# Performance work log

Measured on AMD Instinct MI355X. Metric: run time of the kernel, lower is better.

## Reference

```python
import jax, jax.numpy as jnp
from jax import lax
import numpy as np

B, S, H, DIN, BIN, NH, NL = 32, 256, 256, 16, 2, 8, 3
DH = H // NH


def setup_inputs() -> dict:
    key = jax.random.key(0)
    it = iter(jax.random.split(key, 40))
    def nrm(shape, s=0.05):
        return jax.random.normal(next(it), shape, jnp.float32) * s
    return {
        "parts": jax.random.normal(next(it), (B, S, DIN), jnp.float32),
        "bin_info": jax.random.normal(next(it), (B, BIN), jnp.float32),
        "target": jax.random.randint(next(it), (B, S), 0, S, dtype=jnp.int32),
        "pe_W1": nrm((H // 2, DIN)), "pe_b1": jnp.zeros((H // 2,), jnp.float32),
        "pe_W2": nrm((H // 2, H // 2)), "pe_b2": jnp.zeros((H // 2,), jnp.float32),
        "be_W1": nrm((H // 4, BIN)), "be_b1": jnp.zeros((H // 4,), jnp.float32),
        "be_W2": nrm((H // 4, H // 4)), "be_b2": jnp.zeros((H // 4,), jnp.float32),
        "pos_emb": nrm((S, H // 4)),
        "tr_Wqkv": nrm((NL, 3 * H, H)), "tr_bqkv": jnp.zeros((NL, 3 * H), jnp.float32),
        "tr_Wo": nrm((NL, H, H)), "tr_bo": jnp.zeros((NL, H), jnp.float32),
        "tr_ln1_g": jnp.ones((NL, H), jnp.float32), "tr_ln1_b": jnp.zeros((NL, H), jnp.float32),
        "tr_ff_W1": nrm((NL, 2 * H, H)), "tr_ff_b1": jnp.zeros((NL, 2 * H), jnp.float32),
        "tr_ff_W2": nrm((NL, H, 2 * H)), "tr_ff_b2": jnp.zeros((NL, H), jnp.float32),
        "tr_ln2_g": jnp.ones((NL, H), jnp.float32), "tr_ln2_b": jnp.zeros((NL, H), jnp.float32),
        "lstm_Wih": nrm((4 * H, H)), "lstm_Whh": nrm((4 * H, H)),
        "lstm_bih": jnp.zeros((4 * H,), jnp.float32), "lstm_bhh": jnp.zeros((4 * H,), jnp.float32),
        "ptr_W": nrm((H, H)), "ptr_b": jnp.zeros((H,), jnp.float32),
        "ptr_v": nrm((H,)),
    }


def _ln(x, g, b):
    m = x.mean(-1, keepdims=True)
    v = ((x - m) ** 2).mean(-1, keepdims=True)
    return (x - m) / jnp.sqrt(v + 1e-5) * g + b


def _forward(parts, bin_info, target, pe_W1, pe_b1, pe_W2, pe_b2,
             be_W1, be_b1, be_W2, be_b2, pos_emb,
             tr_Wqkv, tr_bqkv, tr_Wo, tr_bo, tr_ln1_g, tr_ln1_b,
             tr_ff_W1, tr_ff_b1, tr_ff_W2, tr_ff_b2, tr_ln2_g, tr_ln2_b,
             lstm_Wih, lstm_Whh, lstm_bih, lstm_bhh, ptr_W, ptr_b, ptr_v):
    # --- encode_inputs (dropout inactive in eval) ---
    p = jax.nn.relu(parts @ pe_W1.T + pe_b1) @ pe_W2.T + pe_b2            # [B,S,H/2]
    bb = jax.nn.relu(bin_info @ be_W1.T + be_b1) @ be_W2.T + be_b2        # [B,H/4]
    bb = jnp.broadcast_to(bb[:, None, :], (B, S, H // 4))
    pe = jnp.broadcast_to(pos_emb[None], (B, S, H // 4))
    x = jnp.concatenate([p, bb, pe], axis=-1)                             # [B,S,H]
    scale = 1.0 / np.sqrt(DH)
    for l in range(NL):  # post-norm TransformerEncoderLayer, relu FFN
        qkv = x @ tr_Wqkv[l].T + tr_bqkv[l]
        q, k, v = jnp.split(qkv, 3, axis=-1)
        q = q.reshape(B, S, NH, DH).transpose(0, 2, 1, 3)
        k = k.reshape(B, S, NH, DH).transpose(0, 2, 1, 3)
        v = v.reshape(B, S, NH, DH).transpose(0, 2, 1, 3)
        a = jax.nn.softmax(jnp.einsum('bhqd,bhkd->bhqk', q, k) * scale, axis=-1)
        o = jnp.einsum('bhqk,bhkd->bhqd', a, v).transpose(0, 2, 1, 3).reshape(B, S, H)
        x = _ln(x + o @ tr_Wo[l].T + tr_bo[l], tr_ln1_g[l], tr_ln1_b[l])
        ff = jax.nn.relu(x @ tr_ff_W1[l].T + tr_ff_b1[l]) @ tr_ff_W2[l].T + tr_ff_b2[l]
        x = _ln(x + ff, tr_ln2_g[l], tr_ln2_b[l])
    enc = x
    # Note: the original's inner MultiheadAttention calls never feed the
    # returned step_logits (part_logit is overwritten), so the faithful output is
    # logits[b,t,i] = v . tanh(ptr(h_t) + ptr(enc_i)), vectorized over i here.
    e_proj = enc @ ptr_W.T + ptr_b                                        # [B,S,H]
    bidx = jnp.arange(B)

    def step(carry, tgt_t):
        h, c, xin = carry
        g = xin @ lstm_Wih.T + lstm_bih + h @ lstm_Whh.T + lstm_bhh
        i, f, gg, o = jnp.split(g, 4, axis=-1)
        c = jax.nn.sigmoid(f) * c + jax.nn.sigmoid(i) * jnp.tanh(gg)
        h = jax.nn.sigmoid(o) * jnp.tanh(c)
        hp = h @ ptr_W.T + ptr_b                                          # [B,H]
        logits = jnp.tanh(hp[:, None, :] + e_proj) @ ptr_v                # [B,S]
        nxt = enc[bidx, tgt_t]                                            # teacher forcing
        return (h, c, nxt), logits

    z = jnp.zeros((B, H), jnp.float32)
    _, logits = lax.scan(step, (z, z, z), target.T)                       # [S,B,S]
    return logits.transpose(1, 0, 2)                                      # [B,S,S]


def reference(parts, bin_info, target, pe_W1, pe_b1, pe_W2, pe_b2,
              be_W1, be_b1, be_W2, be_b2, pos_emb,
              tr_Wqkv, tr_bqkv, tr_Wo, tr_bo, tr_ln1_g, tr_ln1_b,
              tr_ff_W1, tr_ff_b1, tr_ff_W2, tr_ff_b2, tr_ln2_g, tr_ln2_b,
              lstm_Wih, lstm_Whh, lstm_bih, lstm_bhh, ptr_W, ptr_b, ptr_v):
    return _forward(parts, bin_info, target, pe_W1, pe_b1, pe_W2, pe_b2,
                    be_W1, be_b1, be_W2, be_b2, pos_emb,
                    tr_Wqkv, tr_bqkv, tr_Wo, tr_bo, tr_ln1_g, tr_ln1_b,
                    tr_ff_W1, tr_ff_b1, tr_ff_W2, tr_ff_b2, tr_ln2_g, tr_ln2_b,
                    lstm_Wih, lstm_Whh, lstm_bih, lstm_bhh, ptr_W, ptr_b, ptr_v)
```

## Files before the change

### kernel.cpp

```cpp
#include <hip/hip_runtime.h>
#include <cstddef>

#define DEV __device__ __forceinline__

DEV float fexp2(float x) { return __builtin_amdgcn_exp2f(x); }
DEV float frcp(float x)  { return __builtin_amdgcn_rcpf(x); }
DEV float fsigm(float x) { return frcp(1.0f + fexp2(-1.44269504f * x)); }
DEV float ftanh_(float x){ return 1.0f - 2.0f * frcp(1.0f + fexp2(2.88539008f * x)); }

typedef _Float16 h2t __attribute__((ext_vector_type(2)));
typedef _Float16 v8h __attribute__((ext_vector_type(8)));
typedef float v4f __attribute__((ext_vector_type(4)));
union U32H2 { unsigned int u; h2t h; };
DEV h2t u2h(unsigned int u) { U32H2 x; x.u = u; return x.h; }

template <int BM, int BN, bool RELU, bool OUTF16>
__global__ __launch_bounds__(256) void hgemm_kernel(
    const _Float16* __restrict__ A, const _Float16* __restrict__ W,
    const float* __restrict__ bias1, const float* __restrict__ bias2,
    void* __restrict__ Cout, int M, int N, int K)
{
    constexpr int MT = BM / 32;
    constexpr int NT = BN / 32;
    constexpr int RA = BM / 64;
    constexpr int RB = BN / 64;
    __shared__ _Float16 As[BM * 32];
    __shared__ _Float16 Bs[BN * 32];

    const int tid = threadIdx.x;
    const int lane = tid & 63;
    const int lm = lane & 15, lq = lane >> 4;
    const int wrow = ((tid >> 6) & 1) * (BM / 2);
    const int wcol = (tid >> 7) * (BN / 2);
    const int m0 = blockIdx.x * BM, n0 = blockIdx.y * BN;
    const _Float16* Ab = A + (size_t)m0 * K;
    const _Float16* Wb = W + (size_t)n0 * K;

    v4f acc[MT][NT];
#pragma unroll
    for (int i = 0; i < MT; ++i)
#pragma unroll
        for (int j = 0; j < NT; ++j) acc[i][j] = (v4f){0.f, 0.f, 0.f, 0.f};

    const int rowS = tid >> 2, qS = tid & 3;

    uint4 ra[RA], rb[RB];
#pragma unroll
    for (int r = 0; r < RA; ++r)
        ra[r] = *(const uint4*)(Ab + (size_t)(rowS + 64 * r) * K + qS * 8);
#pragma unroll
    for (int r = 0; r < RB; ++r)
        rb[r] = *(const uint4*)(Wb + (size_t)(rowS + 64 * r) * K + qS * 8);

    for (int k0 = 0; k0 < K; k0 += 32) {
        __syncthreads();
#pragma unroll
        for (int r = 0; r < RA; ++r)
            *(uint4*)(As + (size_t)(tid + 256 * r) * 8) = ra[r];
#pragma unroll
        for (int r = 0; r < RB; ++r)
            *(uint4*)(Bs + (size_t)(tid + 256 * r) * 8) = rb[r];
        __syncthreads();
        int kn = k0 + 32;
        if (kn < K) {
#pragma unroll
            for (int r = 0; r < RA; ++r)
                ra[r] = *(const uint4*)(Ab + (size_t)(rowS + 64 * r) * K + kn + qS * 8);
#pragma unroll
            for (int r = 0; r < RB; ++r)
                rb[r] = *(const uint4*)(Wb + (size_t)(rowS + 64 * r) * K + kn + qS * 8);
        }
        v8h af[MT], bf[NT];
#pragma unroll
        for (int i = 0; i < MT; ++i)
            af[i] = *(const v8h*)(As + (size_t)(wrow + i * 16 + lm) * 32 + lq * 8);
#pragma unroll
        for (int j = 0; j < NT; ++j)
            bf[j] = *(const v8h*)(Bs + (size_t)(wcol + j * 16 + lm) * 32 + lq * 8);
#pragma unroll
        for (int i = 0; i < MT; ++i)
#pragma unroll
            for (int j = 0; j < NT; ++j)
                acc[i][j] = __builtin_amdgcn_mfma_f32_16x16x32_f16(
                    af[i], bf[j], acc[i][j], 0, 0, 0);
    }

#pragma unroll
    for (int j = 0; j < NT; ++j) {
        int col = n0 + wcol + j * 16 + lm;
        float bv = bias1[col];
        if (bias2) bv += bias2[col];
#pragma unroll
        for (int i = 0; i < MT; ++i) {
            int rbase = m0 + wrow + i * 16 + lq * 4;
#pragma unroll
            for (int rg = 0; rg < 4; ++rg) {
                float vv = acc[i][j][rg] + bv;
                if (RELU) vv = fmaxf(vv, 0.f);
                if (OUTF16)
                    ((_Float16*)Cout)[(size_t)(rbase + rg) * N + col] = (_Float16)vv;
                else
                    ((float*)Cout)[(size_t)(rbase + rg) * N + col] = vv;
            }
        }
    }
}

__global__ __launch_bounds__(256) void cvt_all_kernel(
    const float* __restrict__ s0, const float* __restrict__ s1,
    const float* __restrict__ s2, const float* __restrict__ s3,
    const float* __restrict__ s4, const float* __restrict__ s5,
    _Float16* __restrict__ dst)
{
    int i = blockIdx.x * 256 + threadIdx.x;
    if (i >= 1900544) return;
    float val;
    if (i < 589824)       val = s0[i];
    else if (i < 786432)  val = s1[i - 589824];
    else if (i < 1179648) val = s2[i - 786432];
    else if (i < 1572864) val = s3[i - 1179648];
    else if (i < 1835008) {
        int idx = i - 1572864;
        int rp = idx >> 8, k = idx & 255;
        int j = rp >> 2, g = rp & 3;
        val = s4[(g * 256 + j) * 256 + k];
    }
    else                  val = s5[i - 1835008];
    dst[i] = (_Float16)val;
}

__global__ __launch_bounds__(64) void bin_enc_kernel(
    const float* __restrict__ bin_info, const float* __restrict__ W1,
    const float* __restrict__ b1, const float* __restrict__ W2,
    const float* __restrict__ b2, float* __restrict__ BBo)
{
    int b = blockIdx.x, d = threadIdx.x;
    __shared__ float h1[64];
    float x0 = bin_info[b * 2], x1 = bin_info[b * 2 + 1];
    h1[d] = fmaxf(W1[d * 2] * x0 + W1[d * 2 + 1] * x1 + b1[d], 0.f);
    __syncthreads();
    float acc = b2[d];
#pragma unroll 4
    for (int e = 0; e < 64; ++e) acc += W2[d * 64 + e] * h1[e];
    BBo[b * 64 + d] = acc;
}

__global__ __launch_bounds__(128) void part_enc_kernel(
    const float* __restrict__ parts, const float* __restrict__ W1,
    const float* __restrict__ b1, const float* __restrict__ W2,
    const float* __restrict__ b2, const float* __restrict__ BBi,
    const float* __restrict__ pos_emb, float* __restrict__ X,
    _Float16* __restrict__ X16)
{
    __shared__ float W2s[128][129];
    __shared__ float h1[128];
    __shared__ float pin[16];
    int tid = threadIdx.x;
    int b = blockIdx.x >> 3, s0 = (blockIdx.x & 7) * 32;
    for (int l = 0; l < 128; ++l) W2s[l][tid] = W2[l * 128 + tid];
    float w1r[16];
#pragma unroll
    for (int k = 0; k < 16; ++k) w1r[k] = W1[tid * 16 + k];
    float bias1v = b1[tid], bias2v = b2[tid];
    for (int si = 0; si < 32; ++si) {
        int s = s0 + si;
        size_t row = (size_t)b * 256 + s;
        if (tid < 16) pin[tid] = parts[row * 16 + tid];
        __syncthreads();
        float h = bias1v;
#pragma unroll
        for (int k = 0; k < 16; ++k) h += w1r[k] * pin[k];
        h1[tid] = fmaxf(h, 0.f);
        __syncthreads();
        float acc = bias2v;
#pragma unroll 4
        for (int e = 0; e < 128; ++e) acc += W2s[tid][e] * h1[e];
        X[row * 256 + tid] = acc;
        X16[row * 256 + tid] = (_Float16)acc;
        if (tid < 64) {
            float bbv = BBi[b * 64 + tid];
            float pev = pos_emb[s * 64 + tid];
            X[row * 256 + 128 + tid] = bbv;
            X[row * 256 + 192 + tid] = pev;
            X16[row * 256 + 128 + tid] = (_Float16)bbv;
            X16[row * 256 + 192 + tid] = (_Float16)pev;
        }
        __syncthreads();
    }
}

__global__ __launch_bounds__(256) void attn_mfma_kernel(
    const _Float16* __restrict__ QKV, _Float16* __restrict__ O16)
{
    int bh = blockIdx.x;
    int b = bh >> 3, h = bh & 7;
    const int tid = threadIdx.x;
    const int w = tid >> 6;
    const int lane = tid & 63;
    const int lm = lane & 15, lq = lane >> 4;
    const float c_se = 0.17677669529663687f * 1.44269504f;

    __shared__ _Float16 Ks[4][256][8];
    __shared__ _Float16 Vt[32][264];
    __shared__ _Float16 Ps[4][16][264];

    const _Float16* qkvb = QKV + (size_t)(b * 256) * 768 + h * 32;
    {
        int s = tid;
        const _Float16* kr = qkvb + (size_t)s * 768 + 256;
#pragma unroll
        for (int c = 0; c < 4; ++c)
            *(uint4*)&Ks[c][s][0] = *(const uint4*)(kr + c * 8);
        const _Float16* vr = qkvb + (size_t)s * 768 + 512;
        _Float16 vtmp[32];
        *(uint4*)&vtmp[0]  = *(const uint4*)(vr);
        *(uint4*)&vtmp[8]  = *(const uint4*)(vr + 8);
        *(uint4*)&vtmp[16] = *(const uint4*)(vr + 16);
        *(uint4*)&vtmp[24] = *(const uint4*)(vr + 24);
#pragma unroll
        for (int d = 0; d < 32; ++d) Vt[d][s] = vtmp[d];
    }
    __syncthreads();

#pragma unroll 1
    for (int st = 0; st < 4; ++st) {
        int rt = w * 4 + st;
        v8h qf = *(const v8h*)(QKV + (size_t)(b * 256 + rt * 16 + lm) * 768
                               + h * 32 + lq * 8);
        v4f acc[16];
#pragma unroll
        for (int ct = 0; ct < 16; ++ct) {
            v8h kf = *(const v8h*)&Ks[lq][ct * 16 + lm][0];
            acc[ct] = __builtin_amdgcn_mfma_f32_16x16x32_f16(
                qf, kf, (v4f){0.f, 0.f, 0.f, 0.f}, 0, 0, 0);
        }
        float sminv[4];
#pragma unroll
        for (int r = 0; r < 4; ++r) {
            float m = acc[0][r];
#pragma unroll
            for (int ct = 1; ct < 16; ++ct) m = fmaxf(m, acc[ct][r]);
#pragma unroll
            for (int msk = 1; msk < 16; msk <<= 1)
                m = fmaxf(m, __shfl_xor(m, msk));
            float ssum = 0.f;
#pragma unroll
            for (int ct = 0; ct < 16; ++ct) {
                float e = fexp2((acc[ct][r] - m) * c_se);
                acc[ct][r] = e;
                ssum += e;
            }
#pragma unroll
            for (int msk = 1; msk < 16; msk <<= 1)
                ssum += __shfl_xor(ssum, msk);
            sminv[r] = frcp(ssum);
        }
#pragma unroll
        for (int ct = 0; ct < 16; ++ct)
#pragma unroll
            for (int r = 0; r < 4; ++r)
                Ps[w][lq * 4 + r][ct * 16 + lm] =
                    (_Float16)(acc[ct][r] * sminv[r]);
#pragma unroll
        for (int dt = 0; dt < 2; ++dt) {
            v4f o = (v4f){0.f, 0.f, 0.f, 0.f};
#pragma unroll
            for (int jc = 0; jc < 8; ++jc) {
                v8h pf = *(const v8h*)&Ps[w][lm][jc * 32 + lq * 8];
                v8h vf = *(const v8h*)&Vt[dt * 16 + lm][jc * 32 + lq * 8];
                o = __builtin_amdgcn_mfma_f32_16x16x32_f16(pf, vf, o, 0, 0, 0);
            }
#pragma unroll
            for (int r = 0; r < 4; ++r)
                O16[(size_t)(b * 256 + rt * 16 + lq * 4 + r) * 256
                    + h * 32 + dt * 16 + lm] = (_Float16)o[r];
        }
    }
}

__global__ __launch_bounds__(256) void add_ln_kernel(
    float* __restrict__ X, const float* __restrict__ R,
    const float* __restrict__ g, const float* __restrict__ beta,
    _Float16* __restrict__ X16)
{
    int row = blockIdx.x * 4 + (threadIdx.x >> 6);
    int lane = threadIdx.x & 63;
    size_t base = (size_t)row * 256 + lane * 4;
    float4 xv = *(const float4*)&X[base];
    float4 rv = *(const float4*)&R[base];
    float y0 = xv.x + rv.x, y1 = xv.y + rv.y;
    float y2 = xv.z + rv.z, y3 = xv.w + rv.w;
    float s = y0 + y1 + y2 + y3;
    float s2 = y0 * y0 + y1 * y1 + y2 * y2 + y3 * y3;
#pragma unroll
    for (int m = 1; m < 64; m <<= 1) {
        s += __shfl_xor(s, m);
        s2 += __shfl_xor(s2, m);
    }
    float mean = s * (1.f / 256.f);
    float var = s2 * (1.f / 256.f) - mean * mean;
    float inv = rsqrtf(var + 1e-5f);
    float4 gv = *(const float4*)&g[lane * 4];
    float4 bv = *(const float4*)&beta[lane * 4];
    float o0 = (y0 - mean) * inv * gv.x + bv.x;
    float o1 = (y1 - mean) * inv * gv.y + bv.y;
    float o2 = (y2 - mean) * inv * gv.z + bv.z;
    float o3 = (y3 - mean) * inv * gv.w + bv.w;
    *(float4*)&X[base] = make_float4(o0, o1, o2, o3);
    U32H2 a, c;
    a.h = h2t{(_Float16)o0, (_Float16)o1};
    c.h = h2t{(_Float16)o2, (_Float16)o3};
    uint2 u; u.x = a.u; u.y = c.u;
    *(uint2*)(X16 + base) = u;
}

__global__ __launch_bounds__(256) void gather_kernel(
    const float* __restrict__ X, const int* __restrict__ target,
    _Float16* __restrict__ Xg16)
{
    int row = blockIdx.x;
    int b = row >> 8, t = row & 255;
    int d = threadIdx.x;
    float val = 0.f;
    if (t > 0) {
        int src = target[b * 256 + t - 1];
        val = X[((size_t)b * 256 + src) * 256 + d];
    }
    Xg16[(size_t)row * 256 + d] = (_Float16)val;
}

__global__ __launch_bounds__(256) void wcvt2_kernel(
    const float* __restrict__ Whh, unsigned int* __restrict__ WB,
    const float* __restrict__ bih, const float* __restrict__ bhh,
    float* __restrict__ PB)
{
    int idx = blockIdx.x * 256 + threadIdx.x;
    if (idx < 1024) {
        int j = idx >> 2, g = idx & 3;
        PB[idx] = bih[g * 256 + j] + bhh[g * 256 + j];
    }
    int l = idx & 3;
    int gt = idx >> 2;
    int tid = gt & 511;
    int q = gt >> 9;
    int i, c;
    if (q < 8)       { i = q >> 1; c = q & 1; }
    else if (q < 52) { int qq = q - 8; i = qq / 11; c = 2 + qq % 11; }
    else             { int qq = q - 52; c = 13 + (qq >> 2); i = qq & 3; }
    int r = ((tid & 255) << 2) + i;
    int k = ((tid >> 8) << 7) + (c << 3) + (l << 1);
    _Float16 lo = (_Float16)Whh[r * 256 + k];
    _Float16 hi = (_Float16)Whh[r * 256 + k + 1];
    U32H2 x; x.h = h2t{lo, hi};
    WB[idx] = x.u;
}

__global__ __launch_bounds__(512) void lstm_kernel(
    const _Float16* __restrict__ g_in, const uint4* __restrict__ WB4,
    _Float16* __restrict__ HALL16)
{
    const int b = blockIdx.x;
    const int tid = threadIdx.x;
    const int kh = tid >> 8, j4 = tid & 255;

    __shared__ uint4 WL4[4096];
    __shared__ float gpart[2][1024];
    __shared__ uint4 h2v[32];
    unsigned int* h2_s = (unsigned int*)h2v;

#pragma unroll
    for (int g = 0; g < 8; ++g) WL4[g * 512 + tid] = WB4[g * 512 + tid];
    uint4 wr[44];
#pragma unroll
    for (int q = 0; q < 44; ++q) wr[q] = WB4[(8 + q) * 512 + tid];
    if (tid < 128) h2_s[tid] = 0u;

    const _Float16* ginb = g_in + (size_t)b * 256 * 1024;
    uint2 gi = make_uint2(0u, 0u);
    if (tid < 256) gi = *(const uint2*)(ginb + tid * 4);
    float c_state = 0.f;
    const uint4* SW4 = WB4 + 52 * 512;
    __syncthreads();

    for (int t = 0; t < 256; ++t) {
        uint4 sw[12];
#pragma unroll
        for (int q = 0; q < 4; ++q) sw[q] = SW4[q * 512 + tid];

        float acc[4] = {0.f, 0.f, 0.f, 0.f};
#pragma unroll
        for (int c = 0; c < 16; ++c) {
            if (c == 2) {
#pragma unroll
                for (int q = 4; q < 8; ++q) sw[q] = SW4[q * 512 + tid];
            }
            if (c == 6) {
#pragma unroll
                for (int q = 8; q < 12; ++q) sw[q] = SW4[q * 512 + tid];
            }
            uint4 h4 = h2v[(kh << 4) + c];
            h2t hx = u2h(h4.x), hy = u2h(h4.y), hz = u2h(h4.z), hw = u2h(h4.w);
#pragma unroll
            for (int i = 0; i < 4; ++i) {
                uint4 w = (c < 2)  ? WL4[((i << 1) + c) * 512 + tid]
                        : (c < 13) ? wr[i * 11 + (c - 2)]
                                   : sw[((c - 13) << 2) + i];
                acc[i] = __builtin_amdgcn_fdot2(u2h(w.x), hx, acc[i], false);
                acc[i] = __builtin_amdgcn_fdot2(u2h(w.y), hy, acc[i], false);
                acc[i] = __builtin_amdgcn_fdot2(u2h(w.z), hz, acc[i], false);
                acc[i] = __builtin_amdgcn_fdot2(u2h(w.w), hw, acc[i], false);
            }
        }
        *(float4*)&gpart[kh][j4 << 2] = make_float4(acc[0], acc[1], acc[2], acc[3]);
        __syncthreads();

        if (tid < 256) {
            int j = tid;
            h2t p0 = u2h(gi.x), p1 = u2h(gi.y);
            float ig = (float)p0.x + gpart[0][j]       + gpart[1][j];
            float fg = (float)p0.y + gpart[0][j + 256] + gpart[1][j + 256];
            float gg = (float)p1.x + gpart[0][j + 512] + gpart[1][j + 512];
            float og = (float)p1.y + gpart[0][j + 768] + gpart[1][j + 768];
            c_state = fsigm(fg) * c_state + fsigm(ig) * ftanh_(gg);
            float h = fsigm(og) * ftanh_(c_state);
            HALL16[((size_t)(b * 256 + t)) * 256 + j] = (_Float16)h;
            U32H2 hxp; hxp.h = h2t{(_Float16)h, (_Float16)0.f};
            unsigned int hu = hxp.u & 0xffffu;
            unsigned int other = (unsigned int)__shfl_xor((int)hu, 1);
            if ((j & 1) == 0) h2_s[j >> 1] = hu | (other << 16);
            int tn = (t < 255) ? (t + 1) : 255;
            gi = *(const uint2*)(ginb + (size_t)tn * 1024 + j * 4);
        }
        __syncthreads();
    }
}

__global__ __launch_bounds__(256) void pointer_kernel(
    const float* __restrict__ HP, const float* __restrict__ EP,
    const float* __restrict__ v, float* __restrict__ out)
{
    int b = blockIdx.z, tt = blockIdx.y, it = blockIdx.x;
    __shared__ float hp_s[16][260];
    __shared__ float ep_s[16][260];
    __shared__ float v_s[256];
    __shared__ float red[4];
    int tid = threadIdx.x;
    const float cs = 2.88539008f;
    const float* hpb = HP + ((size_t)b * 256 + tt * 16) * 256;
    const float* epb = EP + ((size_t)b * 256 + it * 16) * 256;
#pragma unroll
    for (int l = 0; l < 4; ++l) {
        int idx = tid + l * 256;
        int r = idx >> 6, c4 = idx & 63;
        float4 hv = *(const float4*)(hpb + r * 256 + c4 * 4);
        hv.x *= cs; hv.y *= cs; hv.z *= cs; hv.w *= cs;
        *(float4*)&hp_s[r][c4 * 4] = hv;
        float4 ev = *(const float4*)(epb + r * 256 + c4 * 4);
        ev.x *= cs; ev.y *= cs; ev.z *= cs; ev.w *= cs;
        *(float4*)&ep_s[r][c4 * 4] = ev;
    }
    float vv = v[tid];
    v_s[tid] = vv;
    float vp = vv;
#pragma unroll
    for (int m = 1; m < 64; m <<= 1) vp += __shfl_xor(vp, m);
    if ((tid & 63) == 0) red[tid >> 6] = vp;
    __syncthreads();
    float vsum = red[0] + red[1] + red[2] + red[3];
    int tl = tid >> 4, il = tid & 15;
    float acc = 0.f;
#pragma unroll 4
    for (int d = 0; d < 256; ++d) {
        float sval = hp_s[tl][d] + ep_s[il][d];
        float r = frcp(1.0f + fexp2(sval));
        acc = fmaf(v_s[d], r, acc);
    }
    out[((size_t)b * 256 + tt * 16 + tl) * 256 + it * 16 + il] =
        vsum - 2.0f * acc;
}

extern "C" void kernel_launch(void* const* d_in, const int* in_sizes, int n_in,
                              void* d_out, int out_size, void* d_ws, size_t ws_size,
                              hipStream_t stream)
{
    const float* parts    = (const float*)d_in[0];
    const float* bin_info = (const float*)d_in[1];
    const int*   target   = (const int*)d_in[2];
    const float* pe_W1 = (const float*)d_in[3];
    const float* pe_b1 = (const float*)d_in[4];
    const float* pe_W2 = (const float*)d_in[5];
    const float* pe_b2 = (const float*)d_in[6];
    const float* be_W1 = (const float*)d_in[7];
    const float* be_b1 = (const float*)d_in[8];
    const float* be_W2 = (const float*)d_in[9];
    const float* be_b2 = (const float*)d_in[10];
    const float* pos_emb = (const float*)d_in[11];
    const float* tr_Wqkv = (const float*)d_in[12];
    const float* tr_bqkv = (const float*)d_in[13];
    const float* tr_Wo   = (const float*)d_in[14];
    const float* tr_bo   = (const float*)d_in[15];
    const float* tr_ln1_g = (const float*)d_in[16];
    const float* tr_ln1_b = (const float*)d_in[17];
    const float* tr_ff_W1 = (const float*)d_in[18];
    const float* tr_ff_b1 = (const float*)d_in[19];
    const float* tr_ff_W2 = (const float*)d_in[20];
    const float* tr_ff_b2 = (const float*)d_in[21];
    const float* tr_ln2_g = (const float*)d_in[22];
    const float* tr_ln2_b = (const float*)d_in[23];
    const float* lstm_Wih = (const float*)d_in[24];
    const float* lstm_Whh = (const float*)d_in[25];
    const float* lstm_bih = (const float*)d_in[26];
    const float* lstm_bhh = (const float*)d_in[27];
    const float* ptr_W = (const float*)d_in[28];
    const float* ptr_b = (const float*)d_in[29];
    const float* ptr_v = (const float*)d_in[30];

    float* ws = (float*)d_ws;
    float* X     = ws;
    float* S1    = X + 2097152;
    float* CF32  = S1 + 8388608;
    float* EPROJ = CF32 + 2097152;
    float* X16f  = EPROJ + 2097152;
    float* S2f   = X16f + 1048576;
    float* W16f  = S2f + 1048576;
    float* WBf   = W16f + 1048576;
    float* BBuf  = WBf + 131072;
    float* PB    = BBuf + 2048;

    _Float16* X16    = (_Float16*)X16f;
    _Float16* Xg16   = X16;
    _Float16* S2h    = (_Float16*)S2f;
    _Float16* HALL16 = S2h;
    _Float16* S1h    = (_Float16*)S1;
    _Float16* W16    = (_Float16*)W16f;
    _Float16* Wqkv16 = W16;
    _Float16* Wo16   = Wqkv16 + 589824;
    _Float16* Wff116 = Wo16 + 196608;
    _Float16* Wff216 = Wff116 + 393216;
    _Float16* Wih16  = Wff216 + 393216;
    _Float16* WpW16  = Wih16 + 262144;

    cvt_all_kernel<<<7424, 256, 0, stream>>>(tr_Wqkv, tr_Wo, tr_ff_W1, tr_ff_W2,
                                             lstm_Wih, ptr_W, W16);
    wcvt2_kernel<<<512, 256, 0, stream>>>(lstm_Whh, (unsigned int*)WBf,
                                          lstm_bih, lstm_bhh, PB);

    bin_enc_kernel<<<32, 64, 0, stream>>>(bin_info, be_W1, be_b1, be_W2, be_b2, BBuf);
    part_enc_kernel<<<256, 128, 0, stream>>>(parts, pe_W1, pe_b1, pe_W2, pe_b2,
                                             BBuf, pos_emb, X, X16);

    for (int l = 0; l < 3; ++l) {
        hgemm_kernel<64, 128, false, true><<<dim3(128, 6), 256, 0, stream>>>(
            X16, Wqkv16 + (size_t)l * 196608, tr_bqkv + l * 768, nullptr,
            S1h, 8192, 768, 256);
        attn_mfma_kernel<<<256, 256, 0, stream>>>(S1h, S2h);
        hgemm_kernel<64, 64, false, false><<<dim3(128, 4), 256, 0, stream>>>(
            S2h, Wo16 + (size_t)l * 65536, tr_bo + l * 256, nullptr,
            CF32, 8192, 256, 256);
        add_ln_kernel<<<2048, 256, 0, stream>>>(X, CF32, tr_ln1_g + l * 256,
                                                tr_ln1_b + l * 256, X16);
        hgemm_kernel<64, 128, true, true><<<dim3(128, 4), 256, 0, stream>>>(
            X16, Wff116 + (size_t)l * 131072, tr_ff_b1 + l * 512, nullptr,
            S1h, 8192, 512, 256);
        hgemm_kernel<64, 64, false, false><<<dim3(128, 4), 256, 0, stream>>>(
            S1h, Wff216 + (size_t)l * 131072, tr_ff_b2 + l * 256, nullptr,
            CF32, 8192, 256, 512);
        add_ln_kernel<<<2048, 256, 0, stream>>>(X, CF32, tr_ln2_g + l * 256,
                                                tr_ln2_b + l * 256, X16);
    }

    hgemm_kernel<64, 64, false, false><<<dim3(128, 4), 256, 0, stream>>>(
        X16, WpW16, ptr_b, nullptr, EPROJ, 8192, 256, 256);
    gather_kernel<<<8192, 256, 0, stream>>>(X, target, Xg16);
    hgemm_kernel<64, 128, false, true><<<dim3(128, 8), 256, 0, stream>>>(
        Xg16, Wih16, PB, nullptr, S1h, 8192, 1024, 256);
    lstm_kernel<<<32, 512, 0, stream>>>(S1h, (const uint4*)WBf, HALL16);
    hgemm_kernel<64, 64, false, false><<<dim3(128, 4), 256, 0, stream>>>(
        HALL16, WpW16, ptr_b, nullptr, CF32, 8192, 256, 256);
    pointer_kernel<<<dim3(16, 16, 32), 256, 0, stream>>>(CF32, EPROJ, ptr_v,
                                                         (float*)d_out);
}
```

Before: 1.065 ms.

## Fuse residual+LayerNorm into GEMM epilogue, merge setup kernels, move more LSTM weights to LDS

Adds a full-row (BN=256) MFMA GEMM that applies bias, residual add and LayerNorm in its epilogue. This replaces the separate Wo/FF2 GEMMs and add_ln kernels and removes an fp32 round trip through CF32. The weight-conversion kernels are merged into one launch, and the bin encoder is folded into part_enc. The LSTM keeps more Whh chunks in shared memory (7168 uint4) and reloads fewer per step. The cost is that the fused GEMM runs only 128 blocks, so the GPU has less parallelism for those GEMMs, and the larger LDS footprint in the LSTM kernel.

```diff
diff --git a/kernel.cpp b/kernel.cpp
--- a/kernel.cpp
+++ b/kernel.cpp
@@ -106,58 +106,217 @@
     }
 }
 
-__global__ __launch_bounds__(256) void cvt_all_kernel(
+__global__ __launch_bounds__(256) void hgemm_ln_kernel(
+    const _Float16* __restrict__ A, const _Float16* __restrict__ W,
+    const float* __restrict__ bias, const float* __restrict__ gamma,
+    const float* __restrict__ beta, float* __restrict__ X,
+    _Float16* __restrict__ X16, int K)
+{
+    constexpr int BM = 64, BN = 256, MT = 2, NT = 8, RA = 1, RB = 4;
+    __shared__ _Float16 As[BM * 32];
+    __shared__ _Float16 Bs[BN * 32];
+    __shared__ float redS[2][BM][2];
+
+    const int tid = threadIdx.x;
+    const int lane = tid & 63;
+    const int lm = lane & 15, lq = lane >> 4;
+    const int wrow = ((tid >> 6) & 1) * 32;
+    const int wcol = (tid >> 7) * 128;
+    const int half = tid >> 7;
+    const int m0 = blockIdx.x * BM;
+    const _Float16* Ab = A + (size_t)m0 * K;
+
+    v4f acc[MT][NT];
+#pragma unroll
+    for (int i = 0; i < MT; ++i)
+#pragma unroll
+        for (int j = 0; j < NT; ++j) acc[i][j] = (v4f){0.f, 0.f, 0.f, 0.f};
+
+    const int rowS = tid >> 2, qS = tid & 3;
+
+    uint4 ra[RA], rb[RB];
+#pragma unroll
+    for (int r = 0; r < RA; ++r)
+        ra[r] = *(const uint4*)(Ab + (size_t)(rowS + 64 * r) * K + qS * 8);
+#pragma unroll
+    for (int r = 0; r < RB; ++r)
+        rb[r] = *(const uint4*)(W + (size_t)(rowS + 64 * r) * K + qS * 8);
+
+    for (int k0 = 0; k0 < K; k0 += 32) {
+        __syncthreads();
+#pragma unroll
+        for (int r = 0; r < RA; ++r)
+            *(uint4*)(As + (size_t)(tid + 256 * r) * 8) = ra[r];
+#pragma unroll
+        for (int r = 0; r < RB; ++r)
+            *(uint4*)(Bs + (size_t)(tid + 256 * r) * 8) = rb[r];
+        __syncthreads();
+        int kn = k0 + 32;
+        if (kn < K) {
+#pragma unroll
+            for (int r = 0; r < RA; ++r)
+                ra[r] = *(const uint4*)(Ab + (size_t)(rowS + 64 * r) * K + kn + qS * 8);
+#pragma unroll
+            for (int r = 0; r < RB; ++r)
+                rb[r] = *(const uint4*)(W + (size_t)(rowS + 64 * r) * K + kn + qS * 8);
+        }
+        v8h af[MT], bf[NT];
+#pragma unroll
+        for (int i = 0; i < MT; ++i)
+            af[i] = *(const v8h*)(As + (size_t)(wrow + i * 16 + lm) * 32 + lq * 8);
+#pragma unroll
+        for (int j = 0; j < NT; ++j)
+            bf[j] = *(const v8h*)(Bs + (size_t)(wcol + j * 16 + lm) * 32 + lq * 8);
+#pragma unroll
+        for (int i = 0; i < MT; ++i)
+#pragma unroll
+            for (int j = 0; j < NT; ++j)
+                acc[i][j] = __builtin_amdgcn_mfma_f32_16x16x32_f16(
+                    af[i], bf[j], acc[i][j], 0, 0, 0);
+    }
+
+    float s[MT][4], s2[MT][4];
+#pragma unroll
+    for (int i = 0; i < MT; ++i)
+#pragma unroll
+        for (int rg = 0; rg < 4; ++rg) { s[i][rg] = 0.f; s2[i][rg] = 0.f; }
+#pragma unroll
+    for (int j = 0; j < NT; ++j) {
+        int col = wcol + j * 16 + lm;
+        float bv = bias[col];
+#pragma unroll
+        for (int i = 0; i < MT; ++i) {
+            int rbase = m0 + wrow + i * 16 + lq * 4;
+#pragma unroll
+            for (int rg = 0; rg < 4; ++rg) {
+                float y = acc[i][j][rg] + bv + X[(size_t)(rbase + rg) * 256 + col];
+                acc[i][j][rg] = y;
+                s[i][rg] += y;
+                s2[i][rg] += y * y;
+            }
+        }
+    }
+#pragma unroll
+    for (int i = 0; i < MT; ++i)
+#pragma unroll
+        for (int rg = 0; rg < 4; ++rg) {
+            float a = s[i][rg], b2 = s2[i][rg];
+#pragma unroll
+            for (int m = 1; m < 16; m <<= 1) {
+                a += __shfl_xor(a, m);
+                b2 += __shfl_xor(b2, m);
+            }
+            if (lm == 0) {
+                int rloc = wrow + i * 16 + lq * 4 + rg;
+                redS[half][rloc][0] = a;
+                redS[half][rloc][1] = b2;
+            }
+        }
+    __syncthreads();
+#pragma unroll
+    for (int i = 0; i < MT; ++i) {
+#pragma unroll
+        for (int rg = 0; rg < 4; ++rg) {
+            int rloc = wrow + i * 16 + lq * 4 + rg;
+            float st = redS[0][rloc][0] + redS[1][rloc][0];
+            float s2t = redS[0][rloc][1] + redS[1][rloc][1];
+            float mean = st * (1.f / 256.f);
+            float var = s2t * (1.f / 256.f) - mean * mean;
+            float inv = rsqrtf(var + 1e-5f);
+            size_t rowb = (size_t)(m0 + rloc) * 256;
+#pragma unroll
+            for (int j = 0; j < NT; ++j) {
+                int col = wcol + j * 16 + lm;
+                float o = (acc[i][j][rg] - mean) * inv * gamma[col] + beta[col];
+                X[rowb + col] = o;
+                X16[rowb + col] = (_Float16)o;
+            }
+        }
+    }
+}
+
+__global__ __launch_bounds__(256) void cvt_fused_kernel(
     const float* __restrict__ s0, const float* __restrict__ s1,
     const float* __restrict__ s2, const float* __restrict__ s3,
     const float* __restrict__ s4, const float* __restrict__ s5,
-    _Float16* __restrict__ dst)
-{
-    int i = blockIdx.x * 256 + threadIdx.x;
-    if (i >= 1900544) return;
-    float val;
-    if (i < 589824)       val = s0[i];
-    else if (i < 786432)  val = s1[i - 589824];
-    else if (i < 1179648) val = s2[i - 786432];
-    else if (i < 1572864) val = s3[i - 1179648];
-    else if (i < 1835008) {
-        int idx = i - 1572864;
-        int rp = idx >> 8, k = idx & 255;
-        int j = rp >> 2, g = rp & 3;
-        val = s4[(g * 256 + j) * 256 + k];
-    }
-    else                  val = s5[i - 1835008];
-    dst[i] = (_Float16)val;
-}
-
-__global__ __launch_bounds__(64) void bin_enc_kernel(
-    const float* __restrict__ bin_info, const float* __restrict__ W1,
-    const float* __restrict__ b1, const float* __restrict__ W2,
-    const float* __restrict__ b2, float* __restrict__ BBo)
-{
-    int b = blockIdx.x, d = threadIdx.x;
-    __shared__ float h1[64];
-    float x0 = bin_info[b * 2], x1 = bin_info[b * 2 + 1];
-    h1[d] = fmaxf(W1[d * 2] * x0 + W1[d * 2 + 1] * x1 + b1[d], 0.f);
-    __syncthreads();
-    float acc = b2[d];
-#pragma unroll 4
-    for (int e = 0; e < 64; ++e) acc += W2[d * 64 + e] * h1[e];
-    BBo[b * 64 + d] = acc;
+    _Float16* __restrict__ dst,
+    const float* __restrict__ Whh, unsigned int* __restrict__ WB,
+    const float* __restrict__ bih, const float* __restrict__ bhh,
+    float* __restrict__ PB)
+{
+    if (blockIdx.x < 7424) {
+        int i = blockIdx.x * 256 + threadIdx.x;
+        if (i >= 1900544) return;
+        float val;
+        if (i < 589824)       val = s0[i];
+        else if (i < 786432)  val = s1[i - 589824];
+        else if (i < 1179648) val = s2[i - 786432];
+        else if (i < 1572864) val = s3[i - 1179648];
+        else if (i < 1835008) {
+            int idx = i - 1572864;
+            int rp = idx >> 8, k = idx & 255;
+            int j = rp >> 2, g = rp & 3;
+            val = s4[(g * 256 + j) * 256 + k];
+        }
+        else                  val = s5[i - 1835008];
+        dst[i] = (_Float16)val;
+    } else {
+        int idx = (blockIdx.x - 7424) * 256 + threadIdx.x;
+        if (idx < 1024) {
+            int j = idx >> 2, g = idx & 3;
+            PB[idx] = bih[g * 256 + j] + bhh[g * 256 + j];
+        }
+        int l = idx & 3;
+        int gt = idx >> 2;
+        int tid = gt & 511;
+        int q = gt >> 9;
+        int i, c;
+        if (q < 8)       { i = q >> 1; c = q & 1; }
+        else if (q < 52) { int qq = q - 8; i = qq / 11; c = 2 + qq % 11; }
+        else if (q < 56) { i = q - 52; c = 13; }
+        else if (q < 58) { i = q - 56; c = 14; }
+        else if (q < 60) { i = 2 + (q - 58); c = 14; }
+        else             { i = q - 60; c = 15; }
+        int r = ((tid & 255) << 2) + i;
+        int k = ((tid >> 8) << 7) + (c << 3) + (l << 1);
+        _Float16 lo = (_Float16)Whh[r * 256 + k];
+        _Float16 hi = (_Float16)Whh[r * 256 + k + 1];
+        U32H2 x; x.h = h2t{lo, hi};
+        WB[idx] = x.u;
+    }
 }
 
 __global__ __launch_bounds__(128) void part_enc_kernel(
     const float* __restrict__ parts, const float* __restrict__ W1,
     const float* __restrict__ b1, const float* __restrict__ W2,
-    const float* __restrict__ b2, const float* __restrict__ BBi,
+    const float* __restrict__ b2, const float* __restrict__ bin_info,
+    const float* __restrict__ be_W1, const float* __restrict__ be_b1,
+    const float* __restrict__ be_W2, const float* __restrict__ be_b2,
     const float* __restrict__ pos_emb, float* __restrict__ X,
     _Float16* __restrict__ X16)
 {
     __shared__ float W2s[128][129];
     __shared__ float h1[128];
     __shared__ float pin[16];
+    __shared__ float h1b[64];
+    __shared__ float bb_s[64];
     int tid = threadIdx.x;
     int b = blockIdx.x >> 3, s0 = (blockIdx.x & 7) * 32;
     for (int l = 0; l < 128; ++l) W2s[l][tid] = W2[l * 128 + tid];
+    {
+        float x0 = bin_info[b * 2], x1 = bin_info[b * 2 + 1];
+        if (tid < 64)
+            h1b[tid] = fmaxf(be_W1[tid * 2] * x0 + be_W1[tid * 2 + 1] * x1
+                             + be_b1[tid], 0.f);
+        __syncthreads();
+        if (tid < 64) {
+            float a = be_b2[tid];
+#pragma unroll 4
+            for (int e = 0; e < 64; ++e) a += be_W2[tid * 64 + e] * h1b[e];
+            bb_s[tid] = a;
+        }
+        __syncthreads();
+    }
     float w1r[16];
 #pragma unroll
     for (int k = 0; k < 16; ++k) w1r[k] = W1[tid * 16 + k];
@@ -178,7 +337,7 @@
         X[row * 256 + tid] = acc;
         X16[row * 256 + tid] = (_Float16)acc;
         if (tid < 64) {
-            float bbv = BBi[b * 64 + tid];
+            float bbv = bb_s[tid];
             float pev = pos_emb[s * 64 + tid];
             X[row * 256 + 128 + tid] = bbv;
             X[row * 256 + 192 + tid] = pev;
@@ -278,42 +437,6 @@
     }
 }
 
-__global__ __launch_bounds__(256) void add_ln_kernel(
-    float* __restrict__ X, const float* __restrict__ R,
-    const float* __restrict__ g, const float* __restrict__ beta,
-    _Float16* __restrict__ X16)
-{
-    int row = blockIdx.x * 4 + (threadIdx.x >> 6);
-    int lane = threadIdx.x & 63;
-    size_t base = (size_t)row * 256 + lane * 4;
-    float4 xv = *(const float4*)&X[base];
-    float4 rv = *(const float4*)&R[base];
-    float y0 = xv.x + rv.x, y1 = xv.y + rv.y;
-    float y2 = xv.z + rv.z, y3 = xv.w + rv.w;
-    float s = y0 + y1 + y2 + y3;
-    float s2 = y0 * y0 + y1 * y1 + y2 * y2 + y3 * y3;
-#pragma unroll
-    for (int m = 1; m < 64; m <<= 1) {
-        s += __shfl_xor(s, m);
-        s2 += __shfl_xor(s2, m);
-    }
-    float mean = s * (1.f / 256.f);
-    float var = s2 * (1.f / 256.f) - mean * mean;
-    float inv = rsqrtf(var + 1e-5f);
-    float4 gv = *(const float4*)&g[lane * 4];
-    float4 bv = *(const float4*)&beta[lane * 4];
-    float o0 = (y0 - mean) * inv * gv.x + bv.x;
-    float o1 = (y1 - mean) * inv * gv.y + bv.y;
-    float o2 = (y2 - mean) * inv * gv.z + bv.z;
-    float o3 = (y3 - mean) * inv * gv.w + bv.w;
-    *(float4*)&X[base] = make_float4(o0, o1, o2, o3);
-    U32H2 a, c;
-    a.h = h2t{(_Float16)o0, (_Float16)o1};
-    c.h = h2t{(_Float16)o2, (_Float16)o3};
-    uint2 u; u.x = a.u; u.y = c.u;
-    *(uint2*)(X16 + base) = u;
-}
-
 __global__ __launch_bounds__(256) void gather_kernel(
     const float* __restrict__ X, const int* __restrict__ target,
     _Float16* __restrict__ Xg16)
@@ -329,32 +452,6 @@
     Xg16[(size_t)row * 256 + d] = (_Float16)val;
 }
 
-__global__ __launch_bounds__(256) void wcvt2_kernel(
-    const float* __restrict__ Whh, unsigned int* __restrict__ WB,
-    const float* __restrict__ bih, const float* __restrict__ bhh,
-    float* __restrict__ PB)
-{
-    int idx = blockIdx.x * 256 + threadIdx.x;
-    if (idx < 1024) {
-        int j = idx >> 2, g = idx & 3;
-        PB[idx] = bih[g * 256 + j] + bhh[g * 256 + j];
-    }
-    int l = idx & 3;
-    int gt = idx >> 2;
-    int tid = gt & 511;
-    int q = gt >> 9;
-    int i, c;
-    if (q < 8)       { i = q >> 1; c = q & 1; }
-    else if (q < 52) { int qq = q - 8; i = qq / 11; c = 2 + qq % 11; }
-    else             { int qq = q - 52; c = 13 + (qq >> 2); i = qq & 3; }
-    int r = ((tid & 255) << 2) + i;
-    int k = ((tid >> 8) << 7) + (c << 3) + (l << 1);
-    _Float16 lo = (_Float16)Whh[r * 256 + k];
-    _Float16 hi = (_Float16)Whh[r * 256 + k + 1];
-    U32H2 x; x.h = h2t{lo, hi};
-    WB[idx] = x.u;
-}
-
 __global__ __launch_bounds__(512) void lstm_kernel(
     const _Float16* __restrict__ g_in, const uint4* __restrict__ WB4,
     _Float16* __restrict__ HALL16)
@@ -363,13 +460,16 @@
     const int tid = threadIdx.x;
     const int kh = tid >> 8, j4 = tid & 255;
 
-    __shared__ uint4 WL4[4096];
+    __shared__ uint4 WL4[7168];
     __shared__ float gpart[2][1024];
     __shared__ uint4 h2v[32];
     unsigned int* h2_s = (unsigned int*)h2v;
 
 #pragma unroll
-    for (int g = 0; g < 8; ++g) WL4[g * 512 + tid] = WB4[g * 512 + tid];
+    for (int g = 0; g < 14; ++g) {
+        int src = (g < 8) ? g : (44 + g);
+        WL4[g * 512 + tid] = WB4[src * 512 + tid];
+    }
     uint4 wr[44];
 #pragma unroll
     for (int q = 0; q < 44; ++q) wr[q] = WB4[(8 + q) * 512 + tid];
@@ -379,32 +479,28 @@
     uint2 gi = make_uint2(0u, 0u);
     if (tid < 256) gi = *(const uint2*)(ginb + tid * 4);
     float c_state = 0.f;
-    const uint4* SW4 = WB4 + 52 * 512;
+    const uint4* SW4 = WB4 + 58 * 512;
     __syncthreads();
 
     for (int t = 0; t < 256; ++t) {
-        uint4 sw[12];
-#pragma unroll
-        for (int q = 0; q < 4; ++q) sw[q] = SW4[q * 512 + tid];
+        uint4 sw[6];
+#pragma unroll
+        for (int q = 0; q < 6; ++q) sw[q] = SW4[q * 512 + tid];
 
         float acc[4] = {0.f, 0.f, 0.f, 0.f};
 #pragma unroll
         for (int c = 0; c < 16; ++c) {
-            if (c == 2) {
-#pragma unroll
-                for (int q = 4; q < 8; ++q) sw[q] = SW4[q * 512 + tid];
-            }
-            if (c == 6) {
-#pragma unroll
-                for (int q = 8; q < 12; ++q) sw[q] = SW4[q * 512 + tid];
-            }
             uint4 h4 = h2v[(kh << 4) + c];
             h2t hx = u2h(h4.x), hy = u2h(h4.y), hz = u2h(h4.z), hw = u2h(h4.w);
 #pragma unroll
             for (int i = 0; i < 4; ++i) {
-                uint4 w = (c < 2)  ? WL4[((i << 1) + c) * 512 + tid]
-                        : (c < 13) ? wr[i * 11 + (c - 2)]
-                                   : sw[((c - 13) << 2) + i];
+                uint4 w;
+                if (c < 2)        w = WL4[((i << 1) + c) * 512 + tid];
+                else if (c < 13)  w = wr[i * 11 + (c - 2)];
+                else if (c == 13) w = WL4[(8 + i) * 512 + tid];
+                else if (c == 14) w = (i < 2) ? WL4[(12 + i) * 512 + tid]
+                                              : sw[i - 2];
+                else              w = sw[2 + i];
                 acc[i] = __builtin_amdgcn_fdot2(u2h(w.x), hx, acc[i], false);
                 acc[i] = __builtin_amdgcn_fdot2(u2h(w.y), hy, acc[i], false);
                 acc[i] = __builtin_amdgcn_fdot2(u2h(w.z), hz, acc[i], false);
@@ -540,33 +636,28 @@
     _Float16* Wih16  = Wff216 + 393216;
     _Float16* WpW16  = Wih16 + 262144;
 
-    cvt_all_kernel<<<7424, 256, 0, stream>>>(tr_Wqkv, tr_Wo, tr_ff_W1, tr_ff_W2,
-                                             lstm_Wih, ptr_W, W16);
-    wcvt2_kernel<<<512, 256, 0, stream>>>(lstm_Whh, (unsigned int*)WBf,
-                                          lstm_bih, lstm_bhh, PB);
-
-    bin_enc_kernel<<<32, 64, 0, stream>>>(bin_info, be_W1, be_b1, be_W2, be_b2, BBuf);
+    cvt_fused_kernel<<<7936, 256, 0, stream>>>(
+        tr_Wqkv, tr_Wo, tr_ff_W1, tr_ff_W2, lstm_Wih, ptr_W, W16,
+        lstm_Whh, (unsigned int*)WBf, lstm_bih, lstm_bhh, PB);
+
     part_enc_kernel<<<256, 128, 0, stream>>>(parts, pe_W1, pe_b1, pe_W2, pe_b2,
-                                             BBuf, pos_emb, X, X16);
+                                             bin_info, be_W1, be_b1, be_W2, be_b2,
+                                             pos_emb, X, X16);
 
     for (int l = 0; l < 3; ++l) {
         hgemm_kernel<64, 128, false, true><<<dim3(128, 6), 256, 0, stream>>>(
             X16, Wqkv16 + (size_t)l * 196608, tr_bqkv + l * 768, nullptr,
             S1h, 8192, 768, 256);
         attn_mfma_kernel<<<256, 256, 0, stream>>>(S1h, S2h);
-        hgemm_kernel<64, 64, false, false><<<dim3(128, 4), 256, 0, stream>>>(
-            S2h, Wo16 + (size_t)l * 65536, tr_bo + l * 256, nullptr,
-            CF32, 8192, 256, 256);
-        add_ln_kernel<<<2048, 256, 0, stream>>>(X, CF32, tr_ln1_g + l * 256,
-                                                tr_ln1_b + l * 256, X16);
+        hgemm_ln_kernel<<<128, 256, 0, stream>>>(
+            S2h, Wo16 + (size_t)l * 65536, tr_bo + l * 256,
+            tr_ln1_g + l * 256, tr_ln1_b + l * 256, X, X16, 256);
         hgemm_kernel<64, 128, true, true><<<dim3(128, 4), 256, 0, stream>>>(
             X16, Wff116 + (size_t)l * 131072, tr_ff_b1 + l * 512, nullptr,
             S1h, 8192, 512, 256);
-        hgemm_kernel<64, 64, false, false><<<dim3(128, 4), 256, 0, stream>>>(
-            S1h, Wff216 + (size_t)l * 131072, tr_ff_b2 + l * 256, nullptr,
-            CF32, 8192, 256, 512);
-        add_ln_kernel<<<2048, 256, 0, stream>>>(X, CF32, tr_ln2_g + l * 256,
-                                                tr_ln2_b + l * 256, X16);
+        hgemm_ln_kernel<<<128, 256, 0, stream>>>(
+            S1h, Wff216 + (size_t)l * 131072, tr_ff_b2 + l * 256,
+            tr_ln2_g + l * 256, tr_ln2_b + l * 256, X, X16, 512);
     }
 
     hgemm_kernel<64, 64, false, false><<<dim3(128, 4), 256, 0, stream>>>(
```

After: 1.121 ms. 1.05x slower.
